# Kernel optimization log

Hardware: AMD Instinct MI355X
Metric: run time of the kernel (lower is better)

Reference implementation:

```python
import jax, jax.numpy as jnp
import numpy as np

D_K = 766  # feature dim, also softmax temperature per module init
NEG = -1000000000.0


def setup_inputs() -> dict:
    key = jax.random.key(0)
    k1, k2, k3 = jax.random.split(key, 3)
    B, H, L, D = 2, 4, 2048, D_K
    Q = jax.random.normal(k1, (B, H, L, D), dtype=jnp.float32)
    K = jax.random.normal(k2, (B, H, L, D), dtype=jnp.float32)
    attn_mask = jax.random.randint(k3, (B, H, L, L), 0, 2) > 0  # bool [B,H,Lk,Lq]
    return {"Q": Q, "K": K, "attn_mask": attn_mask}


def reference(Q, K, attn_mask):
    # scores: [B,H,Lq,Lk]
    scores = jnp.einsum("bhqd,bhkd->bhqk", Q, K) / np.sqrt(D_K).astype(np.float32)
    # mask is [B,H,Lk,Lq]; torch applies mask.transpose(2,3)
    scores = jnp.where(jnp.swapaxes(attn_mask, 2, 3), NEG, scores)
    attn1 = jax.nn.softmax(scores, axis=-1)                       # row softmax
    attn2 = jax.nn.softmax(jnp.swapaxes(scores, -1, -2), axis=-1)  # col softmax
    # dropout prob = 0.0 -> identity
    context1 = jnp.einsum("bhqk,bhkd->bhqd", attn1, K)
    context2 = jnp.einsum("bhkq,bhqd->bhkd", attn2, Q)
    return (context1, context2, attn1, attn2)
```

## Files before the change

kernel.cpp:

```cpp
#include <hip/hip_runtime.h>
#include <math.h>

#define L 2048
#define DK 766
#define DKP 768
#define NBH 8
#define NR (NBH * L)
#define NEGV -1000000000.0f

typedef __attribute__((ext_vector_type(8))) short bf16x8_t;
typedef __attribute__((ext_vector_type(4))) float f32x4_t;

#define LDT 72

typedef __attribute__((address_space(1))) const unsigned int gu32;
typedef __attribute__((address_space(3))) unsigned int lu32;

__device__ __forceinline__ short f2bf(float x) {
    union { float f; unsigned u; } v;
    v.f = x;
    unsigned r = v.u + 0x7fff + ((v.u >> 16) & 1);
    return (short)(r >> 16);
}

__device__ __forceinline__ void gl_lds16(const void* g, void* l) {
    __builtin_amdgcn_global_load_lds((gu32*)g, (lu32*)l, 16, 0, 0);
}

__global__ __launch_bounds__(256) void k_cvt2(const float* __restrict__ Q,
                                              const float* __restrict__ K,
                                              short* __restrict__ Qb,
                                              short* __restrict__ Kb) {
    int gid = blockIdx.x * 256 + threadIdx.x;
    const int HALF = 6144 * 256;
    const float* X = (gid < HALF) ? Q : K;
    short* Xb = (gid < HALF) ? Qb : Kb;
    int id = (gid < HALF) ? gid : gid - HALF;
    int row = id / 96, kg = id % 96;
    int k = kg * 8;
    const float* src = &X[(size_t)row * DK + k];
    bf16x8_t v;
#pragma unroll
    for (int p = 0; p < 4; ++p) {
        float2 f = (k + 2 * p < DK) ? *(const float2*)(src + 2 * p)
                                    : make_float2(0.f, 0.f);
        v[2 * p] = f2bf(f.x);
        v[2 * p + 1] = f2bf(f.y);
    }
    *(bf16x8_t*)&Xb[(size_t)row * DKP + k] = v;
}

__global__ __launch_bounds__(256) void k_scoresT(const short* __restrict__ Kb,
                                                 const short* __restrict__ Qb,
                                                 const int* __restrict__ mask,
                                                 float* __restrict__ ST,
                                                 float* __restrict__ prowM,
                                                 float* __restrict__ prowS,
                                                 float* __restrict__ pcolM,
                                                 float* __restrict__ pcolS) {
    __shared__ __align__(16) short As[128 * 64];
    __shared__ __align__(16) short Bs[128 * 64];
    int flat = blockIdx.x + (blockIdx.y << 4) + (blockIdx.z << 8);
    int nw = (flat & 7) * 256 + (flat >> 3);
    const int bxp = nw & 15;
    const int byp = (nw >> 4) & 15;
    const int bh = nw >> 8;

    const short* Am = Kb + (size_t)bh * L * DKP;
    const short* Bm = Qb + (size_t)bh * L * DKP;
    const int* Mm = mask + (size_t)bh * L * L;
    float* Sm = ST + (size_t)bh * L * L;
    const int m0 = byp * 128, n0 = bxp * 128;
    const int t = threadIdx.x, lane = t & 63, wid = t >> 6;
    const int wm = (wid >> 1) * 64, wn = (wid & 1) * 64;
    const int lr = lane & 15, lg = lane >> 4;
    const int lrow = lane >> 3, lcol = lane & 7;

    f32x4_t acc[4][4];
#pragma unroll
    for (int i = 0; i < 4; ++i)
#pragma unroll
        for (int j = 0; j < 4; ++j) acc[i][j] = f32x4_t{0.f, 0.f, 0.f, 0.f};

    for (int k0 = 0; k0 < DKP; k0 += 64) {
#pragma unroll
        for (int g = 0; g < 4; ++g) {
            int row = wid * 32 + g * 8 + lrow;
            gl_lds16(&Am[(size_t)(m0 + row) * DKP + k0 + lcol * 8],
                     (char*)As + wid * 4096 + g * 1024);
            gl_lds16(&Bm[(size_t)(n0 + row) * DKP + k0 + lcol * 8],
                     (char*)Bs + wid * 4096 + g * 1024);
        }
        __syncthreads();
#pragma unroll
        for (int ks = 0; ks < 2; ++ks) {
            bf16x8_t av[4], bv[4];
#pragma unroll
            for (int i = 0; i < 4; ++i)
                av[i] = *(bf16x8_t*)&As[(wm + i * 16 + lr) * 64 + ks * 32 + lg * 8];
#pragma unroll
            for (int j = 0; j < 4; ++j)
                bv[j] = *(bf16x8_t*)&Bs[(wn + j * 16 + lr) * 64 + ks * 32 + lg * 8];
#pragma unroll
            for (int i = 0; i < 4; ++i)
#pragma unroll
                for (int j = 0; j < 4; ++j)
                    acc[i][j] = __builtin_amdgcn_mfma_f32_16x16x32_bf16(
                        av[i], bv[j], acc[i][j], 0, 0, 0);
        }
        __syncthreads();
    }

    const float scale = 1.0f / sqrtf((float)DK);
#pragma unroll
    for (int i = 0; i < 4; ++i) {
        int krow = m0 + wm + i * 16 + lg * 4;
#pragma unroll
        for (int j = 0; j < 4; ++j) {
            int qcol = n0 + wn + j * 16 + lr;
#pragma unroll
            for (int r = 0; r < 4; ++r) {
                int mv = Mm[(size_t)(krow + r) * L + qcol];
                float v = mv ? NEGV : acc[i][j][r] * scale;
                acc[i][j][r] = v;
                Sm[(size_t)(krow + r) * L + qcol] = v;
            }
        }
    }

    float* redb = (float*)As;
#pragma unroll
    for (int i = 0; i < 4; ++i) {
#pragma unroll
        for (int r = 0; r < 4; ++r) {
            float rm = fmaxf(fmaxf(acc[i][0][r], acc[i][1][r]),
                             fmaxf(acc[i][2][r], acc[i][3][r]));
#pragma unroll
            for (int m = 1; m < 16; m <<= 1) rm = fmaxf(rm, __shfl_xor(rm, m, 64));
            float rs = 0.f;
#pragma unroll
            for (int j = 0; j < 4; ++j) rs += expf(acc[i][j][r] - rm);
#pragma unroll
            for (int m = 1; m < 16; m <<= 1) rs += __shfl_xor(rs, m, 64);
            if (lr == 0) {
                int row = wm + i * 16 + lg * 4 + r;
                redb[(wid & 1) * 128 + row] = rm;
                redb[256 + (wid & 1) * 128 + row] = rs;
            }
        }
    }
#pragma unroll
    for (int j = 0; j < 4; ++j) {
        float cm = -INFINITY;
#pragma unroll
        for (int i = 0; i < 4; ++i)
#pragma unroll
            for (int r = 0; r < 4; ++r) cm = fmaxf(cm, acc[i][j][r]);
        cm = fmaxf(cm, __shfl_xor(cm, 16, 64));
        cm = fmaxf(cm, __shfl_xor(cm, 32, 64));
        float cs = 0.f;
#pragma unroll
        for (int i = 0; i < 4; ++i)
#pragma unroll
            for (int r = 0; r < 4; ++r) cs += expf(acc[i][j][r] - cm);
        cs += __shfl_xor(cs, 16, 64);
        cs += __shfl_xor(cs, 32, 64);
        if (lg == 0) {
            int col = wn + j * 16 + lr;
            redb[512 + (wid >> 1) * 128 + col] = cm;
            redb[768 + (wid >> 1) * 128 + col] = cs;
        }
    }
    __syncthreads();
    if (t < 128) {
        float mA = redb[t], mB = redb[128 + t];
        float sA = redb[256 + t], sB = redb[256 + 128 + t];
        float mm = fmaxf(mA, mB);
        float ss = sA * expf(mA - mm) + sB * expf(mB - mm);
        size_t o = (size_t)bxp * NR + bh * L + m0 + t;
        prowM[o] = mm;
        prowS[o] = ss;
    } else {
        int c = t - 128;
        float mA = redb[512 + c], mB = redb[512 + 128 + c];
        float sA = redb[768 + c], sB = redb[768 + 128 + c];
        float mm = fmaxf(mA, mB);
        float ss = sA * expf(mA - mm) + sB * expf(mB - mm);
        size_t o = (size_t)byp * NR + bh * L + n0 + c;
        pcolM[o] = mm;
        pcolS[o] = ss;
    }
}

__global__ __launch_bounds__(256) void k_comb16(const float* __restrict__ prowM,
                                                const float* __restrict__ prowS,
                                                const float* __restrict__ pcolM,
                                                const float* __restrict__ pcolS,
                                                float* __restrict__ m1,
                                                float* __restrict__ r1,
                                                float* __restrict__ m2,
                                                float* __restrict__ r2) {
    int idx = blockIdx.x * 256 + threadIdx.x;
    float m = -INFINITY;
#pragma unroll
    for (int c = 0; c < 16; ++c) m = fmaxf(m, prowM[(size_t)c * NR + idx]);
    float s = 0.f;
#pragma unroll
    for (int c = 0; c < 16; ++c)
        s += prowS[(size_t)c * NR + idx] * expf(prowM[(size_t)c * NR + idx] - m);
    m2[idx] = m;
    r2[idx] = 1.0f / s;

    m = -INFINITY;
#pragma unroll
    for (int c = 0; c < 16; ++c) m = fmaxf(m, pcolM[(size_t)c * NR + idx]);
    s = 0.f;
#pragma unroll
    for (int c = 0; c < 16; ++c)
        s += pcolS[(size_t)c * NR + idx] * expf(pcolM[(size_t)c * NR + idx] - m);
    m1[idx] = m;
    r1[idx] = 1.0f / s;
}

__global__ __launch_bounds__(256) void k_apply(const float* __restrict__ S,
                                               const float* __restrict__ mr,
                                               const float* __restrict__ rr,
                                               const float* __restrict__ mc,
                                               const float* __restrict__ rc,
                                               float* __restrict__ OutIn,
                                               float* __restrict__ OutTr,
                                               short* __restrict__ bIn,
                                               short* __restrict__ bTr) {
    __shared__ float T[64][65];
    const int bh = blockIdx.z;
    const int rb0 = blockIdx.x * 64, cb0 = blockIdx.y * 64;
    const float* Sm = S + (size_t)bh * L * L;
    float* Oin = OutIn + (size_t)bh * L * L;
    float* Otr = OutTr + (size_t)bh * L * L;
    const int t = threadIdx.x, tx = t & 15, ty = t >> 4;

    float4 mcv = *(const float4*)&mc[bh * L + cb0 + tx * 4];
    float4 rcv = *(const float4*)&rc[bh * L + cb0 + tx * 4];

#pragma unroll
    for (int i = 0; i < 4; ++i) {
        int r = rb0 + ty * 4 + i;
        float mrv = mr[bh * L + r], rrv = rr[bh * L + r];
        float4 x = *(const float4*)&Sm[(size_t)r * L + cb0 + tx * 4];
        float4 e = make_float4(expf(x.x - mrv) * rrv, expf(x.y - mrv) * rrv,
                               expf(x.z - mrv) * rrv, expf(x.w - mrv) * rrv);
        *(float4*)&Oin[(size_t)r * L + cb0 + tx * 4] = e;
        short4 b = make_short4(f2bf(e.x), f2bf(e.y), f2bf(e.z), f2bf(e.w));
        *(short4*)&bIn[(size_t)bh * L * L + (size_t)r * L + cb0 + tx * 4] = b;
        T[tx * 4 + 0][ty * 4 + i] = expf(x.x - mcv.x) * rcv.x;
        T[tx * 4 + 1][ty * 4 + i] = expf(x.y - mcv.y) * rcv.y;
        T[tx * 4 + 2][ty * 4 + i] = expf(x.z - mcv.z) * rcv.z;
        T[tx * 4 + 3][ty * 4 + i] = expf(x.w - mcv.w) * rcv.w;
    }
    __syncthreads();
#pragma unroll
    for (int i = 0; i < 4; ++i) {
        int c = ty * 4 + i;
        float4 v = make_float4(T[c][tx * 4], T[c][tx * 4 + 1], T[c][tx * 4 + 2],
                               T[c][tx * 4 + 3]);
        *(float4*)&Otr[(size_t)(cb0 + c) * L + rb0 + tx * 4] = v;
        short4 b = make_short4(f2bf(v.x), f2bf(v.y), f2bf(v.z), f2bf(v.w));
        *(short4*)&bTr[(size_t)bh * L * L + (size_t)(cb0 + c) * L + rb0 + tx * 4] = b;
    }
}

__global__ __launch_bounds__(256) void k_ctx2(const short* __restrict__ a1b,
                                              const short* __restrict__ a2b,
                                              const short* __restrict__ Kb,
                                              const short* __restrict__ Qb,
                                              float* __restrict__ c1,
                                              float* __restrict__ c2) {
    __shared__ __align__(16) short As[128 * 64];
    __shared__ __align__(16) short Bs[128 * LDT];
    int flat = blockIdx.x + blockIdx.y * 6 + blockIdx.z * 96;
    int nw = (flat & 7) * 192 + (flat >> 3);
    int bzp = nw / 96, rem = nw % 96;
    int byp = rem / 6, bxp = rem % 6;
    int bh = bzp & 7;

    const short* Am = ((bzp < 8) ? a1b : a2b) + (size_t)bh * L * L;
    const short* Bm = ((bzp < 8) ? Kb : Qb) + (size_t)bh * L * DKP;
    float* Cm = ((bzp < 8) ? c1 : c2) + (size_t)bh * L * DK;
    const int m0 = byp * 128, n0 = bxp * 128;
    const int t = threadIdx.x, lane = t & 63, wid = t >> 6;
    const int wm = (wid >> 1) * 64, wn = (wid & 1) * 64;
    const int lr = lane & 15, lg = lane >> 4;
    const int lrow = lane >> 3, lcol = lane & 7;

    f32x4_t acc[4][4];
#pragma unroll
    for (int i = 0; i < 4; ++i)
#pragma unroll
        for (int j = 0; j < 4; ++j) acc[i][j] = f32x4_t{0.f, 0.f, 0.f, 0.f};

    for (int k0 = 0; k0 < L; k0 += 64) {
#pragma unroll
        for (int g = 0; g < 4; ++g) {
            int row = wid * 32 + g * 8 + lrow;
            gl_lds16(&Am[(size_t)(m0 + row) * L + k0 + lcol * 8],
                     (char*)As + wid * 4096 + g * 1024);
        }
#pragma unroll
        for (int g = 0; g < 4; ++g) {
            int id = t + 256 * g;
            int d = id & 127, kg = id >> 7;
            const short* src = &Bm[(size_t)(k0 + kg * 8) * DKP + n0 + d];
            bf16x8_t v;
#pragma unroll
            for (int p = 0; p < 8; ++p) v[p] = src[(size_t)p * DKP];
            *(bf16x8_t*)&Bs[d * LDT + kg * 8] = v;
        }
        __syncthreads();
#pragma unroll
        for (int ks = 0; ks < 2; ++ks) {
            bf16x8_t av[4], bv[4];
#pragma unroll
            for (int i = 0; i < 4; ++i)
                av[i] = *(bf16x8_t*)&As[(wm + i * 16 + lr) * 64 + ks * 32 + lg * 8];
#pragma unroll
            for (int j = 0; j < 4; ++j)
                bv[j] = *(bf16x8_t*)&Bs[(wn + j * 16 + lr) * LDT + ks * 32 + lg * 8];
#pragma unroll
            for (int i = 0; i < 4; ++i)
#pragma unroll
                for (int j = 0; j < 4; ++j)
                    acc[i][j] = __builtin_amdgcn_mfma_f32_16x16x32_bf16(
                        av[i], bv[j], acc[i][j], 0, 0, 0);
        }
        __syncthreads();
    }

#pragma unroll
    for (int j = 0; j < 4; ++j) {
        int col = n0 + wn + j * 16 + lr;
        if (col >= DK) continue;
#pragma unroll
        for (int i = 0; i < 4; ++i) {
            int row = m0 + wm + i * 16 + lg * 4;
#pragma unroll
            for (int r = 0; r < 4; ++r)
                Cm[(size_t)(row + r) * DK + col] = acc[i][j][r];
        }
    }
}

extern "C" void kernel_launch(void* const* d_in, const int* in_sizes, int n_in,
                              void* d_out, int out_size, void* d_ws, size_t ws_size,
                              hipStream_t stream) {
    const float* Q = (const float*)d_in[0];
    const float* K = (const float*)d_in[1];
    const int* mask = (const int*)d_in[2];
    float* out = (float*)d_out;

    const size_t CTX = (size_t)NBH * L * DK;
    const size_t ATT = (size_t)NBH * L * L;
    float* c1 = out;
    float* c2 = out + CTX;
    float* a1 = out + 2 * CTX;
    float* a2 = out + 2 * CTX + ATT;

    float* ws = (float*)d_ws;
    float* m1 = ws;
    float* r1 = ws + NR;
    float* m2 = ws + 2 * (size_t)NR;
    float* r2 = ws + 3 * (size_t)NR;
    const size_t QBE = (size_t)NBH * L * DKP;
    short* Qb = (short*)(ws + 4 * (size_t)NR);
    short* Kb = Qb + QBE;
    short* a1b = Kb + QBE;
    short* a2b = a1b + ATT;

    float* prowM = c1;
    float* prowS = c1 + 16 * (size_t)NR;
    float* pcolM = c1 + 32 * (size_t)NR;
    float* pcolS = c1 + 48 * (size_t)NR;

    dim3 blk(256);

    k_cvt2<<<dim3(12288), blk, 0, stream>>>(Q, K, Qb, Kb);
    k_scoresT<<<dim3(16, 16, NBH), blk, 0, stream>>>(Kb, Qb, mask, a2, prowM, prowS,
                                                     pcolM, pcolS);
    k_comb16<<<dim3(NR / 256), blk, 0, stream>>>(prowM, prowS, pcolM, pcolS, m1, r1,
                                                 m2, r2);
    k_apply<<<dim3(32, 32, NBH), blk, 0, stream>>>(a2, m2, r2, m1, r1, a2, a1, a2b,
                                                   a1b);
    k_ctx2<<<dim3(6, 16, 16), blk, 0, stream>>>(a1b, a2b, Kb, Qb, c1, c2);
}
```

Measured before the change: 494.6 us.

## Pre-transpose Q/K to bf16 K-major layout for context GEMMs

```diff
diff --git a/kernel.cpp b/kernel.cpp
--- a/kernel.cpp
+++ b/kernel.cpp
@@ -25,6 +25,49 @@
 
 __device__ __forceinline__ void gl_lds16(const void* g, void* l) {
     __builtin_amdgcn_global_load_lds((gu32*)g, (lu32*)l, 16, 0, 0);
+}
+
+__global__ __launch_bounds__(256) void k_cvtT(const float* __restrict__ Q,
+                                              const float* __restrict__ K,
+                                              short* __restrict__ Qb,
+                                              short* __restrict__ Kb,
+                                              short* __restrict__ Qt,
+                                              short* __restrict__ Kt) {
+    __shared__ short T[64 * LDT];
+    const int tz = blockIdx.z;
+    const int bh = tz & 7;
+    const float* X = (tz < 8) ? Q : K;
+    short* Xb = (tz < 8) ? Qb : Kb;
+    short* Xt = (tz < 8) ? Qt : Kt;
+    X += (size_t)bh * L * DK;
+    Xb += (size_t)bh * L * DKP;
+    Xt += (size_t)bh * DKP * L;
+    const int r0 = blockIdx.y * 64, c0 = blockIdx.x * 64;
+    const int t = threadIdx.x;
+    const int rl = t >> 2, cc = (t & 3) * 16;
+
+    bf16x8_t v0, v1;
+#pragma unroll
+    for (int p = 0; p < 8; ++p) {
+        int c = c0 + cc + 2 * p;
+        float2 f = (c < DK) ? *(const float2*)&X[(size_t)(r0 + rl) * DK + c]
+                            : make_float2(0.f, 0.f);
+        if (p < 4) { v0[2 * p] = f2bf(f.x); v0[2 * p + 1] = f2bf(f.y); }
+        else { v1[2 * (p - 4)] = f2bf(f.x); v1[2 * (p - 4) + 1] = f2bf(f.y); }
+    }
+    *(bf16x8_t*)&Xb[(size_t)(r0 + rl) * DKP + c0 + cc] = v0;
+    *(bf16x8_t*)&Xb[(size_t)(r0 + rl) * DKP + c0 + cc + 8] = v1;
+    *(bf16x8_t*)&T[rl * LDT + cc] = v0;
+    *(bf16x8_t*)&T[rl * LDT + cc + 8] = v1;
+    __syncthreads();
+    bf16x8_t w0, w1;
+#pragma unroll
+    for (int p = 0; p < 8; ++p) {
+        w0[p] = T[(cc + p) * LDT + rl];
+        w1[p] = T[(cc + 8 + p) * LDT + rl];
+    }
+    *(bf16x8_t*)&Xt[(size_t)(c0 + rl) * L + r0 + cc] = w0;
+    *(bf16x8_t*)&Xt[(size_t)(c0 + rl) * L + r0 + cc + 8] = w1;
 }
 
 __global__ __launch_bounds__(256) void k_cvt2(const float* __restrict__ Q,
@@ -269,6 +312,78 @@
     }
 }
 
+__global__ __launch_bounds__(256) void k_ctx2T(const short* __restrict__ a1b,
+                                               const short* __restrict__ a2b,
+                                               const short* __restrict__ Kt,
+                                               const short* __restrict__ Qt,
+                                               float* __restrict__ c1,
+                                               float* __restrict__ c2) {
+    __shared__ __align__(16) short As[128 * 64];
+    __shared__ __align__(16) short Bs[128 * 64];
+    int flat = blockIdx.x + blockIdx.y * 6 + blockIdx.z * 96;
+    int nw = (flat & 7) * 192 + (flat >> 3);
+    int bzp = nw / 96, rem = nw % 96;
+    int byp = rem / 6, bxp = rem % 6;
+    int bh = bzp & 7;
+
+    const short* Am = ((bzp < 8) ? a1b : a2b) + (size_t)bh * L * L;
+    const short* Bt = ((bzp < 8) ? Kt : Qt) + (size_t)bh * DKP * L;
+    float* Cm = ((bzp < 8) ? c1 : c2) + (size_t)bh * L * DK;
+    const int m0 = byp * 128, n0 = bxp * 128;
+    const int t = threadIdx.x, lane = t & 63, wid = t >> 6;
+    const int wm = (wid >> 1) * 64, wn = (wid & 1) * 64;
+    const int lr = lane & 15, lg = lane >> 4;
+    const int lrow = lane >> 3, lcol = lane & 7;
+
+    f32x4_t acc[4][4];
+#pragma unroll
+    for (int i = 0; i < 4; ++i)
+#pragma unroll
+        for (int j = 0; j < 4; ++j) acc[i][j] = f32x4_t{0.f, 0.f, 0.f, 0.f};
+
+    for (int k0 = 0; k0 < L; k0 += 64) {
+#pragma unroll
+        for (int g = 0; g < 4; ++g) {
+            int row = wid * 32 + g * 8 + lrow;
+            gl_lds16(&Am[(size_t)(m0 + row) * L + k0 + lcol * 8],
+                     (char*)As + wid * 4096 + g * 1024);
+            gl_lds16(&Bt[(size_t)(n0 + row) * L + k0 + lcol * 8],
+                     (char*)Bs + wid * 4096 + g * 1024);
+        }
+        __syncthreads();
+#pragma unroll
+        for (int ks = 0; ks < 2; ++ks) {
+            bf16x8_t av[4], bv[4];
+#pragma unroll
+            for (int i = 0; i < 4; ++i)
+                av[i] = *(bf16x8_t*)&As[(wm + i * 16 + lr) * 64 + ks * 32 + lg * 8];
+#pragma unroll
+            for (int j = 0; j < 4; ++j)
+                bv[j] = *(bf16x8_t*)&Bs[(wn + j * 16 + lr) * 64 + ks * 32 + lg * 8];
+#pragma unroll
+            for (int i = 0; i < 4; ++i)
+#pragma unroll
+                for (int j = 0; j < 4; ++j)
+                    acc[i][j] = __builtin_amdgcn_mfma_f32_16x16x32_bf16(
+                        av[i], bv[j], acc[i][j], 0, 0, 0);
+        }
+        __syncthreads();
+    }
+
+#pragma unroll
+    for (int j = 0; j < 4; ++j) {
+        int col = n0 + wn + j * 16 + lr;
+        if (col >= DK) continue;
+#pragma unroll
+        for (int i = 0; i < 4; ++i) {
+            int row = m0 + wm + i * 16 + lg * 4;
+#pragma unroll
+            for (int r = 0; r < 4; ++r)
+                Cm[(size_t)(row + r) * DK + col] = acc[i][j][r];
+        }
+    }
+}
+
 __global__ __launch_bounds__(256) void k_ctx2(const short* __restrict__ a1b,
                                               const short* __restrict__ a2b,
                                               const short* __restrict__ Kb,
@@ -374,6 +489,10 @@
     short* Kb = Qb + QBE;
     short* a1b = Kb + QBE;
     short* a2b = a1b + ATT;
+    short* Qt = a2b + ATT;
+    short* Kt = Qt + QBE;
+
+    const size_t NEED_T = 4 * (size_t)NR * 4 + (4 * QBE + 2 * ATT) * 2;
 
     float* prowM = c1;
     float* prowS = c1 + 16 * (size_t)NR;
@@ -381,13 +500,22 @@
     float* pcolS = c1 + 48 * (size_t)NR;
 
     dim3 blk(256);
-
-    k_cvt2<<<dim3(12288), blk, 0, stream>>>(Q, K, Qb, Kb);
+    const bool fast = (ws_size >= NEED_T);
+
+    if (fast) {
+        k_cvtT<<<dim3(12, 32, 16), blk, 0, stream>>>(Q, K, Qb, Kb, Qt, Kt);
+    } else {
+        k_cvt2<<<dim3(12288), blk, 0, stream>>>(Q, K, Qb, Kb);
+    }
     k_scoresT<<<dim3(16, 16, NBH), blk, 0, stream>>>(Kb, Qb, mask, a2, prowM, prowS,
                                                      pcolM, pcolS);
     k_comb16<<<dim3(NR / 256), blk, 0, stream>>>(prowM, prowS, pcolM, pcolS, m1, r1,
                                                  m2, r2);
     k_apply<<<dim3(32, 32, NBH), blk, 0, stream>>>(a2, m2, r2, m1, r1, a2, a1, a2b,
                                                    a1b);
-    k_ctx2<<<dim3(6, 16, 16), blk, 0, stream>>>(a1b, a2b, Kb, Qb, c1, c2);
-}
+    if (fast) {
+        k_ctx2T<<<dim3(6, 16, 16), blk, 0, stream>>>(a1b, a2b, Kt, Qt, c1, c2);
+    } else {
+        k_ctx2<<<dim3(6, 16, 16), blk, 0, stream>>>(a1b, a2b, Kb, Qb, c1, c2);
+    }
+}
```

New measurement: 528.4 us. +6.8%, slower.

## Pre-transpose Q/K in convert kernel and rewrite context GEMM with 256x256 pipelined tiles

Applied to the files above, without the earlier changes.

```diff
diff --git a/kernel.cpp b/kernel.cpp
--- a/kernel.cpp
+++ b/kernel.cpp
@@ -27,27 +27,52 @@
     __builtin_amdgcn_global_load_lds((gu32*)g, (lu32*)l, 16, 0, 0);
 }
 
-__global__ __launch_bounds__(256) void k_cvt2(const float* __restrict__ Q,
+#define BARR() asm volatile("s_barrier" ::: "memory")
+#define VMW() asm volatile("s_waitcnt vmcnt(0)" ::: "memory")
+#define PRIO1() __builtin_amdgcn_s_setprio(1)
+#define PRIO0() __builtin_amdgcn_s_setprio(0)
+
+__global__ __launch_bounds__(256) void k_cvtT(const float* __restrict__ Q,
                                               const float* __restrict__ K,
                                               short* __restrict__ Qb,
-                                              short* __restrict__ Kb) {
-    int gid = blockIdx.x * 256 + threadIdx.x;
-    const int HALF = 6144 * 256;
-    const float* X = (gid < HALF) ? Q : K;
-    short* Xb = (gid < HALF) ? Qb : Kb;
-    int id = (gid < HALF) ? gid : gid - HALF;
-    int row = id / 96, kg = id % 96;
-    int k = kg * 8;
-    const float* src = &X[(size_t)row * DK + k];
-    bf16x8_t v;
-#pragma unroll
-    for (int p = 0; p < 4; ++p) {
-        float2 f = (k + 2 * p < DK) ? *(const float2*)(src + 2 * p)
-                                    : make_float2(0.f, 0.f);
-        v[2 * p] = f2bf(f.x);
-        v[2 * p + 1] = f2bf(f.y);
-    }
-    *(bf16x8_t*)&Xb[(size_t)row * DKP + k] = v;
+                                              short* __restrict__ Kb,
+                                              short* __restrict__ Qt,
+                                              short* __restrict__ Kt) {
+    __shared__ short T[64 * LDT];
+    const int tz = blockIdx.z;
+    const int bh = tz & 7;
+    const float* X = (tz < 8) ? Q : K;
+    short* Xb = (tz < 8) ? Qb : Kb;
+    short* Xt = (tz < 8) ? Qt : Kt;
+    X += (size_t)bh * L * DK;
+    Xb += (size_t)bh * L * DKP;
+    Xt += (size_t)bh * DKP * L;
+    const int r0 = blockIdx.y * 64, c0 = blockIdx.x * 64;
+    const int t = threadIdx.x;
+    const int rl = t >> 2, cc = (t & 3) * 16;
+
+    bf16x8_t v0, v1;
+#pragma unroll
+    for (int p = 0; p < 8; ++p) {
+        int c = c0 + cc + 2 * p;
+        float2 f = (c < DK) ? *(const float2*)&X[(size_t)(r0 + rl) * DK + c]
+                            : make_float2(0.f, 0.f);
+        if (p < 4) { v0[2 * p] = f2bf(f.x); v0[2 * p + 1] = f2bf(f.y); }
+        else { v1[2 * (p - 4)] = f2bf(f.x); v1[2 * (p - 4) + 1] = f2bf(f.y); }
+    }
+    *(bf16x8_t*)&Xb[(size_t)(r0 + rl) * DKP + c0 + cc] = v0;
+    *(bf16x8_t*)&Xb[(size_t)(r0 + rl) * DKP + c0 + cc + 8] = v1;
+    *(bf16x8_t*)&T[rl * LDT + cc] = v0;
+    *(bf16x8_t*)&T[rl * LDT + cc + 8] = v1;
+    __syncthreads();
+    bf16x8_t w0, w1;
+#pragma unroll
+    for (int p = 0; p < 8; ++p) {
+        w0[p] = T[(cc + p) * LDT + rl];
+        w1[p] = T[(cc + 8 + p) * LDT + rl];
+    }
+    *(bf16x8_t*)&Xt[(size_t)(c0 + rl) * L + r0 + cc] = w0;
+    *(bf16x8_t*)&Xt[(size_t)(c0 + rl) * L + r0 + cc + 8] = w1;
 }
 
 __global__ __launch_bounds__(256) void k_scoresT(const short* __restrict__ Kb,
@@ -269,84 +294,134 @@
     }
 }
 
-__global__ __launch_bounds__(256) void k_ctx2(const short* __restrict__ a1b,
-                                              const short* __restrict__ a2b,
-                                              const short* __restrict__ Kb,
-                                              const short* __restrict__ Qb,
-                                              float* __restrict__ c1,
-                                              float* __restrict__ c2) {
-    __shared__ __align__(16) short As[128 * 64];
-    __shared__ __align__(16) short Bs[128 * LDT];
-    int flat = blockIdx.x + blockIdx.y * 6 + blockIdx.z * 96;
-    int nw = (flat & 7) * 192 + (flat >> 3);
-    int bzp = nw / 96, rem = nw % 96;
-    int byp = rem / 6, bxp = rem % 6;
-    int bh = bzp & 7;
-
-    const short* Am = ((bzp < 8) ? a1b : a2b) + (size_t)bh * L * L;
-    const short* Bm = ((bzp < 8) ? Kb : Qb) + (size_t)bh * L * DKP;
-    float* Cm = ((bzp < 8) ? c1 : c2) + (size_t)bh * L * DK;
-    const int m0 = byp * 128, n0 = bxp * 128;
+__global__ __launch_bounds__(512, 2) void k_ctx8(const short* __restrict__ a1b,
+                                                 const short* __restrict__ a2b,
+                                                 const short* __restrict__ Kt,
+                                                 const short* __restrict__ Qt,
+                                                 float* __restrict__ c1,
+                                                 float* __restrict__ c2) {
+    __shared__ __align__(16) short LB[65536];
+
+    int flat = blockIdx.x;
+    int nw = (flat & 7) * 48 + (flat >> 3);
+    int inst = nw / 24, rem = nw % 24;
+    int myp = rem / 3, nxp = rem % 3;
+    int bh = inst & 7;
+    const short* Am = ((inst < 8) ? a1b : a2b) + (size_t)bh * L * L;
+    const short* Bt = ((inst < 8) ? Kt : Qt) + (size_t)bh * DKP * L;
+    float* Cm = ((inst < 8) ? c1 : c2) + (size_t)bh * L * DK;
+    const int m0 = myp * 256, n0 = nxp * 256;
+
     const int t = threadIdx.x, lane = t & 63, wid = t >> 6;
-    const int wm = (wid >> 1) * 64, wn = (wid & 1) * 64;
+    const int wr = wid >> 2, wc = wid & 3;
     const int lr = lane & 15, lg = lane >> 4;
-    const int lrow = lane >> 3, lcol = lane & 7;
-
-    f32x4_t acc[4][4];
-#pragma unroll
-    for (int i = 0; i < 4; ++i)
+
+    const int schunk = (lane & 7) ^ (lane >> 3);
+    const short* aSrc = Am + (size_t)(m0 + wid * 8 + (lane >> 3)) * L + schunk * 8;
+    const short* bSrc = Bt + (size_t)(n0 + wid * 8 + (lane >> 3)) * L + schunk * 8;
+    char* ldsA = (char*)LB;
+    char* ldsB = (char*)LB + 65536;
+
+#define STAGEA(cb, k0n)                                                              \
+    do {                                                                             \
+        gl_lds16(aSrc + (k0n), ldsA + (cb)*32768 + wid * 1024);                      \
+        gl_lds16(aSrc + (size_t)64 * L + (k0n), ldsA + (cb)*32768 + 8192 + wid * 1024); \
+        gl_lds16(aSrc + (size_t)128 * L + (k0n), ldsA + (cb)*32768 + 16384 + wid * 1024); \
+        gl_lds16(aSrc + (size_t)192 * L + (k0n), ldsA + (cb)*32768 + 24576 + wid * 1024); \
+    } while (0)
+#define STAGEB(cb, k0n)                                                              \
+    do {                                                                             \
+        gl_lds16(bSrc + (k0n), ldsB + (cb)*32768 + wid * 1024);                      \
+        gl_lds16(bSrc + (size_t)64 * L + (k0n), ldsB + (cb)*32768 + 8192 + wid * 1024); \
+        gl_lds16(bSrc + (size_t)128 * L + (k0n), ldsB + (cb)*32768 + 16384 + wid * 1024); \
+        gl_lds16(bSrc + (size_t)192 * L + (k0n), ldsB + (cb)*32768 + 24576 + wid * 1024); \
+    } while (0)
+
+    const int axr = lr & 7;
+    const int kc0 = ((0 + lg) ^ axr) * 8;
+    const int kc1 = ((4 + lg) ^ axr) * 8;
+    const int aRd = wr * 8192 + lr * 64;
+    const int bRd = 32768 + (wc >> 1) * 8192 + ((wc & 1) * 64 + lr) * 64;
+
+#define LDA0(c, i) (*(const bf16x8_t*)&LB[(c)*16384 + aRd + (i)*1024 + kc0])
+#define LDA1(c, i) (*(const bf16x8_t*)&LB[(c)*16384 + aRd + (i)*1024 + kc1])
+#define LDB0(c, j) (*(const bf16x8_t*)&LB[(c)*16384 + bRd + (j)*1024 + kc0])
+#define LDB1(c, j) (*(const bf16x8_t*)&LB[(c)*16384 + bRd + (j)*1024 + kc1])
+
+    f32x4_t acc[8][4];
+#pragma unroll
+    for (int i = 0; i < 8; ++i)
 #pragma unroll
         for (int j = 0; j < 4; ++j) acc[i][j] = f32x4_t{0.f, 0.f, 0.f, 0.f};
 
-    for (int k0 = 0; k0 < L; k0 += 64) {
-#pragma unroll
-        for (int g = 0; g < 4; ++g) {
-            int row = wid * 32 + g * 8 + lrow;
-            gl_lds16(&Am[(size_t)(m0 + row) * L + k0 + lcol * 8],
-                     (char*)As + wid * 4096 + g * 1024);
-        }
-#pragma unroll
-        for (int g = 0; g < 4; ++g) {
-            int id = t + 256 * g;
-            int d = id & 127, kg = id >> 7;
-            const short* src = &Bm[(size_t)(k0 + kg * 8) * DKP + n0 + d];
-            bf16x8_t v;
-#pragma unroll
-            for (int p = 0; p < 8; ++p) v[p] = src[(size_t)p * DKP];
-            *(bf16x8_t*)&Bs[d * LDT + kg * 8] = v;
-        }
-        __syncthreads();
-#pragma unroll
-        for (int ks = 0; ks < 2; ++ks) {
-            bf16x8_t av[4], bv[4];
-#pragma unroll
-            for (int i = 0; i < 4; ++i)
-                av[i] = *(bf16x8_t*)&As[(wm + i * 16 + lr) * 64 + ks * 32 + lg * 8];
-#pragma unroll
-            for (int j = 0; j < 4; ++j)
-                bv[j] = *(bf16x8_t*)&Bs[(wn + j * 16 + lr) * LDT + ks * 32 + lg * 8];
-#pragma unroll
-            for (int i = 0; i < 4; ++i)
-#pragma unroll
-                for (int j = 0; j < 4; ++j)
-                    acc[i][j] = __builtin_amdgcn_mfma_f32_16x16x32_bf16(
-                        av[i], bv[j], acc[i][j], 0, 0, 0);
-        }
-        __syncthreads();
-    }
-
-#pragma unroll
-    for (int j = 0; j < 4; ++j) {
-        int col = n0 + wn + j * 16 + lr;
-        if (col >= DK) continue;
-#pragma unroll
-        for (int i = 0; i < 4; ++i) {
-            int row = m0 + wm + i * 16 + lg * 4;
-#pragma unroll
-            for (int r = 0; r < 4; ++r)
-                Cm[(size_t)(row + r) * DK + col] = acc[i][j][r];
-        }
-    }
+    bf16x8_t bfr[4][2];
+
+#define PHASE(c, i0, EXTRA)                                                          \
+    do {                                                                             \
+        bf16x8_t a00 = LDA0(c, i0), a01 = LDA1(c, i0);                               \
+        bf16x8_t a10 = LDA0(c, (i0) + 1), a11 = LDA1(c, (i0) + 1);                   \
+        EXTRA;                                                                       \
+        BARR();                                                                      \
+        PRIO1();                                                                     \
+        _Pragma("unroll") for (int j = 0; j < 4; ++j) {                              \
+            acc[i0][j] = __builtin_amdgcn_mfma_f32_16x16x32_bf16(a00, bfr[j][0],     \
+                                                                 acc[i0][j], 0, 0, 0); \
+            acc[i0][j] = __builtin_amdgcn_mfma_f32_16x16x32_bf16(a01, bfr[j][1],     \
+                                                                 acc[i0][j], 0, 0, 0); \
+            acc[(i0) + 1][j] = __builtin_amdgcn_mfma_f32_16x16x32_bf16(              \
+                a10, bfr[j][0], acc[(i0) + 1][j], 0, 0, 0);                          \
+            acc[(i0) + 1][j] = __builtin_amdgcn_mfma_f32_16x16x32_bf16(              \
+                a11, bfr[j][1], acc[(i0) + 1][j], 0, 0, 0);                          \
+        }                                                                            \
+        PRIO0();                                                                     \
+    } while (0)
+
+    const int NT = L / 64;
+    STAGEA(0, 0);
+    STAGEB(0, 0);
+    VMW();
+    BARR();
+
+    for (int kt = 0; kt < NT; ++kt) {
+        const int c = kt & 1;
+        const bool ds = (kt + 1 < NT);
+        const int k0n = (kt + 1) * 64;
+#pragma unroll
+        for (int j = 0; j < 4; ++j) {
+            bfr[j][0] = LDB0(c, j);
+            bfr[j][1] = LDB1(c, j);
+        }
+        PHASE(c, 0, if (ds) STAGEA(c ^ 1, k0n));
+        BARR();
+        PHASE(c, 2, if (ds) STAGEB(c ^ 1, k0n));
+        BARR();
+        PHASE(c, 4, ((void)0));
+        BARR();
+        PHASE(c, 6, ((void)0));
+        if (ds) VMW();
+        BARR();
+    }
+
+#pragma unroll
+    for (int i = 0; i < 8; ++i) {
+        int row = m0 + wr * 128 + i * 16 + lg * 4;
+#pragma unroll
+        for (int j = 0; j < 4; ++j) {
+            int col = n0 + wc * 64 + j * 16 + lr;
+            if (col < DK) {
+#pragma unroll
+                for (int r = 0; r < 4; ++r)
+                    Cm[(size_t)(row + r) * DK + col] = acc[i][j][r];
+            }
+        }
+    }
+#undef PHASE
+#undef STAGEA
+#undef STAGEB
+#undef LDA0
+#undef LDA1
+#undef LDB0
+#undef LDB1
 }
 
 extern "C" void kernel_launch(void* const* d_in, const int* in_sizes, int n_in,
@@ -374,6 +449,8 @@
     short* Kb = Qb + QBE;
     short* a1b = Kb + QBE;
     short* a2b = a1b + ATT;
+    short* Qt = a2b + ATT;
+    short* Kt = Qt + QBE;
 
     float* prowM = c1;
     float* prowS = c1 + 16 * (size_t)NR;
@@ -382,12 +459,12 @@
 
     dim3 blk(256);
 
-    k_cvt2<<<dim3(12288), blk, 0, stream>>>(Q, K, Qb, Kb);
+    k_cvtT<<<dim3(12, 32, 16), blk, 0, stream>>>(Q, K, Qb, Kb, Qt, Kt);
     k_scoresT<<<dim3(16, 16, NBH), blk, 0, stream>>>(Kb, Qb, mask, a2, prowM, prowS,
                                                      pcolM, pcolS);
     k_comb16<<<dim3(NR / 256), blk, 0, stream>>>(prowM, prowS, pcolM, pcolS, m1, r1,
                                                  m2, r2);
     k_apply<<<dim3(32, 32, NBH), blk, 0, stream>>>(a2, m2, r2, m1, r1, a2, a1, a2b,
                                                    a1b);
-    k_ctx2<<<dim3(6, 16, 16), blk, 0, stream>>>(a1b, a2b, Kb, Qb, c1, c2);
-}
+    k_ctx8<<<dim3(384), dim3(512), 0, stream>>>(a1b, a2b, Kt, Qt, c1, c2);
+}
```

After: 477.9 us. 1.03x faster.
